# Performance work log

Hardware: AMD Instinct MI355X
Metric: run time of the kernel (lower is better)

## Reference

```python
import jax, jax.numpy as jnp
import numpy as np

B, T, I, H, L, C = 256, 512, 128, 256, 2, 1000


def _uniform(key, shape, k):
    return jax.random.uniform(key, shape, jnp.float32, -k, k)


def setup_inputs() -> dict:
    key = jax.random.key(0)
    ks = jax.random.split(key, 12)
    k = 1.0 / np.sqrt(H)
    return {
        "x": jax.random.normal(ks[0], (B, T, I), jnp.float32),
        # layer 0 (PyTorch LSTM param layout: W_ih [4H, in], W_hh [4H, H], biases [4H])
        "Wih0": _uniform(ks[1], (4 * H, I), k),
        "Whh0": _uniform(ks[2], (4 * H, H), k),
        "bih0": _uniform(ks[3], (4 * H,), k),
        "bhh0": _uniform(ks[4], (4 * H,), k),
        # layer 1
        "Wih1": _uniform(ks[5], (4 * H, H), k),
        "Whh1": _uniform(ks[6], (4 * H, H), k),
        "bih1": _uniform(ks[7], (4 * H,), k),
        "bhh1": _uniform(ks[8], (4 * H,), k),
        # final classifier
        "fcW": _uniform(ks[9], (C, H), k),
        "fcb": _uniform(ks[10], (C,), k),
    }


def _lstm_layer(seq, Wih, Whh, bias):
    # seq: [B, T, in]; returns hidden sequence [B, T, H]
    b, t = seq.shape[0], seq.shape[1]
    h_dim = Whh.shape[1]
    # Precompute input projection for all timesteps (one big GEMM).
    x_proj = jnp.einsum('bti,gi->btg', seq, Wih) + bias  # [B, T, 4H]

    def step(carry, xp):
        h, c = carry
        gates = xp + h @ Whh.T                     # [B, 4H]
        i, f, g, o = jnp.split(gates, 4, axis=-1)  # PyTorch gate order i,f,g,o
        i = jax.nn.sigmoid(i)
        f = jax.nn.sigmoid(f)
        g = jnp.tanh(g)
        o = jax.nn.sigmoid(o)
        c = f * c + i * g
        h = o * jnp.tanh(c)
        return (h, c), h

    h0 = jnp.zeros((b, h_dim), seq.dtype)
    c0 = jnp.zeros((b, h_dim), seq.dtype)
    _, hs = jax.lax.scan(step, (h0, c0), jnp.swapaxes(x_proj, 0, 1))  # [T, B, H]
    return jnp.swapaxes(hs, 0, 1)


def reference(x, Wih0, Whh0, bih0, bhh0, Wih1, Whh1, bih1, bhh1, fcW, fcb):
    out = _lstm_layer(x, Wih0, Whh0, bih0 + bhh0)
    out = _lstm_layer(out, Wih1, Whh1, bih1 + bhh1)
    # classifier on last timestep
    return out[:, -1, :] @ fcW.T + fcb  # [B, C]
```

## Files before the change

kernel.cpp:

```cpp
#include <hip/hip_runtime.h>

#define B_ 256
#define T_ 512
#define I_ 128
#define H_ 256
#define C_ 1000

__device__ __forceinline__ float fsig(float x) { return 1.0f / (1.0f + __expf(-x)); }
__device__ __forceinline__ float ftanh(float x) { return 2.0f / (1.0f + __expf(-2.0f * x)) - 1.0f; }

__global__ __launch_bounds__(256) void lstm_step(
    const float* __restrict__ x,
    const float* __restrict__ Wih0, const float* __restrict__ Whh0,
    const float* __restrict__ bih0, const float* __restrict__ bhh0,
    const float* __restrict__ Wih1, const float* __restrict__ Whh1,
    const float* __restrict__ bih1, const float* __restrict__ bhh1,
    float* __restrict__ ws, int s)
{
    __shared__ float As[128 * 36];
    __shared__ float Wsh[128 * 36];

    float* h0buf = ws;
    float* h1buf = ws + 2 * B_ * H_;
    float* c0 = ws + 4 * B_ * H_;
    float* c1 = ws + 5 * B_ * H_;

    const int w = blockIdx.x;
    const int layer = w >> 8;
    const int r = w & 255;
    const int bb = r >> 5;
    const int hb = r & 31;

    if (layer == 0 && s >= T_) return;
    if (layer == 1 && s < 1) return;
    const int t = (layer == 0) ? s : (s - 1);

    const float* hprev; const float* h0cur = nullptr;
    float* hout; float* cbuf;
    const float* Wih; const float* Whh; const float* bi; const float* bh;
    int nchunks;
    if (layer == 0) {
        hprev = h0buf + ((t - 1) & 1) * B_ * H_;
        hout  = h0buf + (t & 1) * B_ * H_;
        cbuf = c0; Wih = Wih0; Whh = Whh0; bi = bih0; bh = bhh0;
        nchunks = 3;
    } else {
        h0cur = h0buf + (t & 1) * B_ * H_;
        hprev = h1buf + ((t - 1) & 1) * B_ * H_;
        hout  = h1buf + (t & 1) * B_ * H_;
        cbuf = c1; Wih = Wih1; Whh = Whh1; bi = bih1; bh = bhh1;
        nchunks = 4;
    }

    const int tid = threadIdx.x;
    const int srow = tid >> 3;
    const int kv = tid & 7;
    const int wave = tid >> 6;
    const int lane = tid & 63;
    const int br = lane >> 3;
    const int gc8 = lane & 7;
    const int grow = (srow >> 3) * H_ + hb * 8 + (srow & 7);

    float acc[4][4];
#pragma unroll
    for (int a = 0; a < 4; ++a)
#pragma unroll
        for (int b = 0; b < 4; ++b) acc[a][b] = 0.0f;

    for (int cc = 0; cc < nchunks; ++cc) {
        const float* ap;
        const float* wp;
        if (layer == 0) {
            if (cc == 0) { ap = x + ((size_t)(bb * 32 + srow) * T_ + t) * I_; wp = Wih + grow * I_; }
            else         { ap = hprev + (bb * 32 + srow) * H_ + (cc - 1) * 128; wp = Whh + grow * H_ + (cc - 1) * 128; }
        } else {
            if (cc < 2)  { ap = h0cur + (bb * 32 + srow) * H_ + cc * 128;       wp = Wih + grow * H_ + cc * 128; }
            else         { ap = hprev + (bb * 32 + srow) * H_ + (cc - 2) * 128; wp = Whh + grow * H_ + (cc - 2) * 128; }
        }
#pragma unroll
        for (int i = 0; i < 4; ++i) {
            const int k4 = (kv + 8 * i) * 4;
            float4 va = *(const float4*)(ap + k4);
            As[(k4 + 0) * 36 + srow] = va.x;
            As[(k4 + 1) * 36 + srow] = va.y;
            As[(k4 + 2) * 36 + srow] = va.z;
            As[(k4 + 3) * 36 + srow] = va.w;
            float4 vw = *(const float4*)(wp + k4);
            Wsh[(k4 + 0) * 36 + srow] = vw.x;
            Wsh[(k4 + 1) * 36 + srow] = vw.y;
            Wsh[(k4 + 2) * 36 + srow] = vw.z;
            Wsh[(k4 + 3) * 36 + srow] = vw.w;
        }
        __syncthreads();
        const float* Ap = &As[(wave * 32) * 36 + br * 4];
        const float* Wp = &Wsh[(wave * 32) * 36 + gc8 * 4];
#pragma unroll
        for (int kk = 0; kk < 32; ++kk) {
            float4 a = *(const float4*)(Ap + kk * 36);
            float4 wv = *(const float4*)(Wp + kk * 36);
            acc[0][0] += a.x * wv.x; acc[0][1] += a.x * wv.y; acc[0][2] += a.x * wv.z; acc[0][3] += a.x * wv.w;
            acc[1][0] += a.y * wv.x; acc[1][1] += a.y * wv.y; acc[1][2] += a.y * wv.z; acc[1][3] += a.y * wv.w;
            acc[2][0] += a.z * wv.x; acc[2][1] += a.z * wv.y; acc[2][2] += a.z * wv.z; acc[2][3] += a.z * wv.w;
            acc[3][0] += a.w * wv.x; acc[3][1] += a.w * wv.y; acc[3][2] += a.w * wv.z; acc[3][3] += a.w * wv.w;
        }
        __syncthreads();
    }

    float* red = As;
    {
        const int base = tid * 16;
#pragma unroll
        for (int a = 0; a < 4; ++a)
#pragma unroll
            for (int b = 0; b < 4; ++b)
                red[base + a * 4 + b] = acc[a][b];
    }
    __syncthreads();
    {
        const int bl = tid >> 3;
        const int j = tid & 7;
        float g4[4];
#pragma unroll
        for (int g = 0; g < 4; ++g) {
            const int gc = g * 8 + j;
            const int br2 = bl >> 2, bi2 = bl & 3, gq = gc >> 2, gj = gc & 3;
            float v = 0.0f;
#pragma unroll
            for (int wv = 0; wv < 4; ++wv)
                v += red[(wv * 64 + br2 * 8 + gq) * 16 + bi2 * 4 + gj];
            const int growg = g * H_ + hb * 8 + j;
            v += bi[growg] + bh[growg];
            g4[g] = v;
        }
        const float ig = fsig(g4[0]);
        const float fg = fsig(g4[1]);
        const float gg = ftanh(g4[2]);
        const float og = fsig(g4[3]);
        const int b = bb * 32 + bl;
        const int hidx = hb * 8 + j;
        const int ci = b * H_ + hidx;
        const float cn = fg * cbuf[ci] + ig * gg;
        cbuf[ci] = cn;
        hout[ci] = og * ftanh(cn);
    }
}

__global__ __launch_bounds__(256) void fc_kernel(
    const float* __restrict__ ws, const float* __restrict__ fcW,
    const float* __restrict__ fcb, float* __restrict__ out)
{
    __shared__ float As[128 * 36];
    __shared__ float Wsh[128 * 36];

    const float* h1 = ws + 3 * B_ * H_;
    const int bb = blockIdx.x >> 5;
    const int cb = blockIdx.x & 31;
    const int tid = threadIdx.x;
    const int srow = tid >> 3;
    const int kv = tid & 7;
    const int wave = tid >> 6;
    const int lane = tid & 63;
    const int br = lane >> 3;
    const int gc8 = lane & 7;
    const int crow = cb * 32 + srow;

    float acc[4][4];
#pragma unroll
    for (int a = 0; a < 4; ++a)
#pragma unroll
        for (int b = 0; b < 4; ++b) acc[a][b] = 0.0f;

    for (int cc = 0; cc < 2; ++cc) {
        const float* ap = h1 + (bb * 32 + srow) * H_ + cc * 128;
#pragma unroll
        for (int i = 0; i < 4; ++i) {
            const int k4 = (kv + 8 * i) * 4;
            float4 va = *(const float4*)(ap + k4);
            As[(k4 + 0) * 36 + srow] = va.x;
            As[(k4 + 1) * 36 + srow] = va.y;
            As[(k4 + 2) * 36 + srow] = va.z;
            As[(k4 + 3) * 36 + srow] = va.w;
            float4 vw = make_float4(0.f, 0.f, 0.f, 0.f);
            if (crow < C_) vw = *(const float4*)(fcW + crow * H_ + cc * 128 + k4);
            Wsh[(k4 + 0) * 36 + srow] = vw.x;
            Wsh[(k4 + 1) * 36 + srow] = vw.y;
            Wsh[(k4 + 2) * 36 + srow] = vw.z;
            Wsh[(k4 + 3) * 36 + srow] = vw.w;
        }
        __syncthreads();
        const float* Ap = &As[(wave * 32) * 36 + br * 4];
        const float* Wp = &Wsh[(wave * 32) * 36 + gc8 * 4];
#pragma unroll
        for (int kk = 0; kk < 32; ++kk) {
            float4 a = *(const float4*)(Ap + kk * 36);
            float4 wv = *(const float4*)(Wp + kk * 36);
            acc[0][0] += a.x * wv.x; acc[0][1] += a.x * wv.y; acc[0][2] += a.x * wv.z; acc[0][3] += a.x * wv.w;
            acc[1][0] += a.y * wv.x; acc[1][1] += a.y * wv.y; acc[1][2] += a.y * wv.z; acc[1][3] += a.y * wv.w;
            acc[2][0] += a.z * wv.x; acc[2][1] += a.z * wv.y; acc[2][2] += a.z * wv.z; acc[2][3] += a.z * wv.w;
            acc[3][0] += a.w * wv.x; acc[3][1] += a.w * wv.y; acc[3][2] += a.w * wv.z; acc[3][3] += a.w * wv.w;
        }
        __syncthreads();
    }

    float* red = As;
    {
        const int base = tid * 16;
#pragma unroll
        for (int a = 0; a < 4; ++a)
#pragma unroll
            for (int b = 0; b < 4; ++b)
                red[base + a * 4 + b] = acc[a][b];
    }
    __syncthreads();
    {
        const int bl = tid >> 3;
        const int j = tid & 7;
#pragma unroll
        for (int g = 0; g < 4; ++g) {
            const int gc = g * 8 + j;
            const int br2 = bl >> 2, bi2 = bl & 3, gq = gc >> 2, gj = gc & 3;
            float v = 0.0f;
#pragma unroll
            for (int wv = 0; wv < 4; ++wv)
                v += red[(wv * 64 + br2 * 8 + gq) * 16 + bi2 * 4 + gj];
            const int cglob = cb * 32 + gc;
            if (cglob < C_) {
                v += fcb[cglob];
                out[(size_t)(bb * 32 + bl) * C_ + cglob] = v;
            }
        }
    }
}

extern "C" void kernel_launch(void* const* d_in, const int* in_sizes, int n_in,
                              void* d_out, int out_size, void* d_ws, size_t ws_size,
                              hipStream_t stream)
{
    const float* x    = (const float*)d_in[0];
    const float* Wih0 = (const float*)d_in[1];
    const float* Whh0 = (const float*)d_in[2];
    const float* bih0 = (const float*)d_in[3];
    const float* bhh0 = (const float*)d_in[4];
    const float* Wih1 = (const float*)d_in[5];
    const float* Whh1 = (const float*)d_in[6];
    const float* bih1 = (const float*)d_in[7];
    const float* bhh1 = (const float*)d_in[8];
    const float* fcW  = (const float*)d_in[9];
    const float* fcb  = (const float*)d_in[10];
    float* ws  = (float*)d_ws;
    float* out = (float*)d_out;

    hipMemsetAsync(d_ws, 0, (size_t)6 * B_ * H_ * sizeof(float), stream);

    for (int s = 0; s <= T_; ++s) {
        lstm_step<<<512, 256, 0, stream>>>(x, Wih0, Whh0, bih0, bhh0,
                                           Wih1, Whh1, bih1, bhh1, ws, s);
    }
    fc_kernel<<<256, 256, 0, stream>>>(ws, fcW, fcb, out);
}
```

Measured before the change: 7.486 ms.

## Replace per-timestep kernel launches with persistent kernel and per-batch-group barriers

Merges the 513 per-step launches and the classifier launch into one persistent kernel of 512 blocks. Blocks sharing a batch group sync through an atomic counter barrier with sleep polling, and hidden state is passed through agent-scope atomic loads and stores. This removes launch overhead and the device-wide step boundary, so batch groups can run ahead independently. The cost is that all 512 blocks must be co-resident, which relies on 2 blocks per CU, or the kernel deadlocks. It also adds spin overhead and relaxed-ordering risks.

Measured after the change: 8.458 ms. +13.0%, slower.

```diff
diff --git a/kernel.cpp b/kernel.cpp
--- a/kernel.cpp
+++ b/kernel.cpp
@@ -9,13 +9,23 @@
 __device__ __forceinline__ float fsig(float x) { return 1.0f / (1.0f + __expf(-x)); }
 __device__ __forceinline__ float ftanh(float x) { return 2.0f / (1.0f + __expf(-2.0f * x)) - 1.0f; }
 
-__global__ __launch_bounds__(256) void lstm_step(
+__device__ __forceinline__ float4 load_f4_coh(const float* p) {
+    unsigned long long* q = (unsigned long long*)p;
+    unsigned long long a = __hip_atomic_load(&q[0], __ATOMIC_RELAXED, __HIP_MEMORY_SCOPE_AGENT);
+    unsigned long long b = __hip_atomic_load(&q[1], __ATOMIC_RELAXED, __HIP_MEMORY_SCOPE_AGENT);
+    union { unsigned long long u; float f[2]; } ua, ub;
+    ua.u = a; ub.u = b;
+    return make_float4(ua.f[0], ua.f[1], ub.f[0], ub.f[1]);
+}
+
+__global__ __launch_bounds__(256, 2) void lstm_persistent(
     const float* __restrict__ x,
     const float* __restrict__ Wih0, const float* __restrict__ Whh0,
     const float* __restrict__ bih0, const float* __restrict__ bhh0,
     const float* __restrict__ Wih1, const float* __restrict__ Whh1,
     const float* __restrict__ bih1, const float* __restrict__ bhh1,
-    float* __restrict__ ws, int s)
+    const float* __restrict__ fcW, const float* __restrict__ fcb,
+    float* __restrict__ ws, float* __restrict__ out)
 {
     __shared__ float As[128 * 36];
     __shared__ float Wsh[128 * 36];
@@ -24,33 +34,14 @@
     float* h1buf = ws + 2 * B_ * H_;
     float* c0 = ws + 4 * B_ * H_;
     float* c1 = ws + 5 * B_ * H_;
+    unsigned* cnts = (unsigned*)(ws + 6 * B_ * H_);
 
     const int w = blockIdx.x;
     const int layer = w >> 8;
     const int r = w & 255;
     const int bb = r >> 5;
     const int hb = r & 31;
-
-    if (layer == 0 && s >= T_) return;
-    if (layer == 1 && s < 1) return;
-    const int t = (layer == 0) ? s : (s - 1);
-
-    const float* hprev; const float* h0cur = nullptr;
-    float* hout; float* cbuf;
-    const float* Wih; const float* Whh; const float* bi; const float* bh;
-    int nchunks;
-    if (layer == 0) {
-        hprev = h0buf + ((t - 1) & 1) * B_ * H_;
-        hout  = h0buf + (t & 1) * B_ * H_;
-        cbuf = c0; Wih = Wih0; Whh = Whh0; bi = bih0; bh = bhh0;
-        nchunks = 3;
-    } else {
-        h0cur = h0buf + (t & 1) * B_ * H_;
-        hprev = h1buf + ((t - 1) & 1) * B_ * H_;
-        hout  = h1buf + (t & 1) * B_ * H_;
-        cbuf = c1; Wih = Wih1; Whh = Whh1; bi = bih1; bh = bhh1;
-        nchunks = 4;
-    }
+    unsigned* cnt = cnts + bb * 64;
 
     const int tid = threadIdx.x;
     const int srow = tid >> 3;
@@ -61,172 +52,198 @@
     const int gc8 = lane & 7;
     const int grow = (srow >> 3) * H_ + hb * 8 + (srow & 7);
 
-    float acc[4][4];
-#pragma unroll
-    for (int a = 0; a < 4; ++a)
-#pragma unroll
-        for (int b = 0; b < 4; ++b) acc[a][b] = 0.0f;
-
-    for (int cc = 0; cc < nchunks; ++cc) {
-        const float* ap;
-        const float* wp;
-        if (layer == 0) {
-            if (cc == 0) { ap = x + ((size_t)(bb * 32 + srow) * T_ + t) * I_; wp = Wih + grow * I_; }
-            else         { ap = hprev + (bb * 32 + srow) * H_ + (cc - 1) * 128; wp = Whh + grow * H_ + (cc - 1) * 128; }
-        } else {
-            if (cc < 2)  { ap = h0cur + (bb * 32 + srow) * H_ + cc * 128;       wp = Wih + grow * H_ + cc * 128; }
-            else         { ap = hprev + (bb * 32 + srow) * H_ + (cc - 2) * 128; wp = Whh + grow * H_ + (cc - 2) * 128; }
-        }
-#pragma unroll
-        for (int i = 0; i < 4; ++i) {
-            const int k4 = (kv + 8 * i) * 4;
-            float4 va = *(const float4*)(ap + k4);
-            As[(k4 + 0) * 36 + srow] = va.x;
-            As[(k4 + 1) * 36 + srow] = va.y;
-            As[(k4 + 2) * 36 + srow] = va.z;
-            As[(k4 + 3) * 36 + srow] = va.w;
-            float4 vw = *(const float4*)(wp + k4);
-            Wsh[(k4 + 0) * 36 + srow] = vw.x;
-            Wsh[(k4 + 1) * 36 + srow] = vw.y;
-            Wsh[(k4 + 2) * 36 + srow] = vw.z;
-            Wsh[(k4 + 3) * 36 + srow] = vw.w;
-        }
+    const float* Wih = layer ? Wih1 : Wih0;
+    const float* Whh = layer ? Whh1 : Whh0;
+    const float* bi  = layer ? bih1 : bih0;
+    const float* bh  = layer ? bhh1 : bhh0;
+    const int nchunks = layer ? 4 : 3;
+
+    for (int s = 0; s <= T_; ++s) {
+        const bool active = layer ? (s >= 1) : (s < T_);
+        if (active) {
+            const int t = layer ? (s - 1) : s;
+            const float* hprev;
+            const float* h0cur = nullptr;
+            float* hout;
+            float* cbuf;
+            if (layer == 0) {
+                hprev = h0buf + ((t - 1) & 1) * B_ * H_;
+                hout  = h0buf + (t & 1) * B_ * H_;
+                cbuf = c0;
+            } else {
+                h0cur = h0buf + (t & 1) * B_ * H_;
+                hprev = h1buf + ((t - 1) & 1) * B_ * H_;
+                hout  = h1buf + (t & 1) * B_ * H_;
+                cbuf = c1;
+            }
+
+            float acc[4][4];
+#pragma unroll
+            for (int a = 0; a < 4; ++a)
+#pragma unroll
+                for (int b = 0; b < 4; ++b) acc[a][b] = 0.0f;
+
+            for (int cc = 0; cc < nchunks; ++cc) {
+                const float* ap;
+                const float* wp;
+                bool ap_coherent = true;
+                if (layer == 0) {
+                    if (cc == 0) { ap = x + ((size_t)(bb * 32 + srow) * T_ + t) * I_; wp = Wih + grow * I_; ap_coherent = false; }
+                    else         { ap = hprev + (bb * 32 + srow) * H_ + (cc - 1) * 128; wp = Whh + grow * H_ + (cc - 1) * 128; }
+                } else {
+                    if (cc < 2)  { ap = h0cur + (bb * 32 + srow) * H_ + cc * 128;       wp = Wih + grow * H_ + cc * 128; }
+                    else         { ap = hprev + (bb * 32 + srow) * H_ + (cc - 2) * 128; wp = Whh + grow * H_ + (cc - 2) * 128; }
+                }
+#pragma unroll
+                for (int i = 0; i < 4; ++i) {
+                    const int k4 = (kv + 8 * i) * 4;
+                    float4 va = ap_coherent ? load_f4_coh(ap + k4) : *(const float4*)(ap + k4);
+                    As[(k4 + 0) * 36 + srow] = va.x;
+                    As[(k4 + 1) * 36 + srow] = va.y;
+                    As[(k4 + 2) * 36 + srow] = va.z;
+                    As[(k4 + 3) * 36 + srow] = va.w;
+                    float4 vw = *(const float4*)(wp + k4);
+                    Wsh[(k4 + 0) * 36 + srow] = vw.x;
+                    Wsh[(k4 + 1) * 36 + srow] = vw.y;
+                    Wsh[(k4 + 2) * 36 + srow] = vw.z;
+                    Wsh[(k4 + 3) * 36 + srow] = vw.w;
+                }
+                __syncthreads();
+                const float* Ap = &As[(wave * 32) * 36 + br * 4];
+                const float* Wp = &Wsh[(wave * 32) * 36 + gc8 * 4];
+#pragma unroll
+                for (int kk = 0; kk < 32; ++kk) {
+                    float4 a = *(const float4*)(Ap + kk * 36);
+                    float4 wv = *(const float4*)(Wp + kk * 36);
+                    acc[0][0] += a.x * wv.x; acc[0][1] += a.x * wv.y; acc[0][2] += a.x * wv.z; acc[0][3] += a.x * wv.w;
+                    acc[1][0] += a.y * wv.x; acc[1][1] += a.y * wv.y; acc[1][2] += a.y * wv.z; acc[1][3] += a.y * wv.w;
+                    acc[2][0] += a.z * wv.x; acc[2][1] += a.z * wv.y; acc[2][2] += a.z * wv.z; acc[2][3] += a.z * wv.w;
+                    acc[3][0] += a.w * wv.x; acc[3][1] += a.w * wv.y; acc[3][2] += a.w * wv.z; acc[3][3] += a.w * wv.w;
+                }
+                __syncthreads();
+            }
+
+            float* red = As;
+            {
+                const int base = tid * 16;
+#pragma unroll
+                for (int a = 0; a < 4; ++a)
+#pragma unroll
+                    for (int b = 0; b < 4; ++b)
+                        red[base + a * 4 + b] = acc[a][b];
+            }
+            __syncthreads();
+            {
+                const int bl = tid >> 3;
+                const int j = tid & 7;
+                float g4[4];
+#pragma unroll
+                for (int g = 0; g < 4; ++g) {
+                    const int gc = g * 8 + j;
+                    const int br2 = bl >> 2, bi2 = bl & 3, gq = gc >> 2, gj = gc & 3;
+                    float v = 0.0f;
+#pragma unroll
+                    for (int wv = 0; wv < 4; ++wv)
+                        v += red[(wv * 64 + br2 * 8 + gq) * 16 + bi2 * 4 + gj];
+                    const int growg = g * H_ + hb * 8 + j;
+                    v += bi[growg] + bh[growg];
+                    g4[g] = v;
+                }
+                const float ig = fsig(g4[0]);
+                const float fg = fsig(g4[1]);
+                const float gg = ftanh(g4[2]);
+                const float og = fsig(g4[3]);
+                const int b = bb * 32 + bl;
+                const int hidx = hb * 8 + j;
+                const int ci = b * H_ + hidx;
+                const float cn = fg * cbuf[ci] + ig * gg;
+                cbuf[ci] = cn;
+                __hip_atomic_store(&hout[ci], og * ftanh(cn),
+                                   __ATOMIC_RELAXED, __HIP_MEMORY_SCOPE_AGENT);
+            }
+            __syncthreads();
+        }
+
         __syncthreads();
-        const float* Ap = &As[(wave * 32) * 36 + br * 4];
-        const float* Wp = &Wsh[(wave * 32) * 36 + gc8 * 4];
-#pragma unroll
-        for (int kk = 0; kk < 32; ++kk) {
-            float4 a = *(const float4*)(Ap + kk * 36);
-            float4 wv = *(const float4*)(Wp + kk * 36);
-            acc[0][0] += a.x * wv.x; acc[0][1] += a.x * wv.y; acc[0][2] += a.x * wv.z; acc[0][3] += a.x * wv.w;
-            acc[1][0] += a.y * wv.x; acc[1][1] += a.y * wv.y; acc[1][2] += a.y * wv.z; acc[1][3] += a.y * wv.w;
-            acc[2][0] += a.z * wv.x; acc[2][1] += a.z * wv.y; acc[2][2] += a.z * wv.z; acc[2][3] += a.z * wv.w;
-            acc[3][0] += a.w * wv.x; acc[3][1] += a.w * wv.y; acc[3][2] += a.w * wv.z; acc[3][3] += a.w * wv.w;
+        if (tid == 0) {
+            __hip_atomic_fetch_add(cnt, 1u, __ATOMIC_RELAXED, __HIP_MEMORY_SCOPE_AGENT);
+            const unsigned target = (unsigned)(s + 1) * 64u;
+            while (__hip_atomic_load(cnt, __ATOMIC_RELAXED, __HIP_MEMORY_SCOPE_AGENT) < target) {
+                __builtin_amdgcn_s_sleep(2);
+            }
         }
         __syncthreads();
     }
 
-    float* red = As;
-    {
-        const int base = tid * 16;
+    if (layer == 1) {
+        const int cb = hb;
+        const float* h1 = ws + 3 * B_ * H_;
+        const int crow = cb * 32 + srow;
+
+        float acc[4][4];
 #pragma unroll
         for (int a = 0; a < 4; ++a)
 #pragma unroll
-            for (int b = 0; b < 4; ++b)
-                red[base + a * 4 + b] = acc[a][b];
-    }
-    __syncthreads();
-    {
-        const int bl = tid >> 3;
-        const int j = tid & 7;
-        float g4[4];
-#pragma unroll
-        for (int g = 0; g < 4; ++g) {
-            const int gc = g * 8 + j;
-            const int br2 = bl >> 2, bi2 = bl & 3, gq = gc >> 2, gj = gc & 3;
-            float v = 0.0f;
-#pragma unroll
-            for (int wv = 0; wv < 4; ++wv)
-                v += red[(wv * 64 + br2 * 8 + gq) * 16 + bi2 * 4 + gj];
-            const int growg = g * H_ + hb * 8 + j;
-            v += bi[growg] + bh[growg];
-            g4[g] = v;
-        }
-        const float ig = fsig(g4[0]);
-        const float fg = fsig(g4[1]);
-        const float gg = ftanh(g4[2]);
-        const float og = fsig(g4[3]);
-        const int b = bb * 32 + bl;
-        const int hidx = hb * 8 + j;
-        const int ci = b * H_ + hidx;
-        const float cn = fg * cbuf[ci] + ig * gg;
-        cbuf[ci] = cn;
-        hout[ci] = og * ftanh(cn);
-    }
-}
-
-__global__ __launch_bounds__(256) void fc_kernel(
-    const float* __restrict__ ws, const float* __restrict__ fcW,
-    const float* __restrict__ fcb, float* __restrict__ out)
-{
-    __shared__ float As[128 * 36];
-    __shared__ float Wsh[128 * 36];
-
-    const float* h1 = ws + 3 * B_ * H_;
-    const int bb = blockIdx.x >> 5;
-    const int cb = blockIdx.x & 31;
-    const int tid = threadIdx.x;
-    const int srow = tid >> 3;
-    const int kv = tid & 7;
-    const int wave = tid >> 6;
-    const int lane = tid & 63;
-    const int br = lane >> 3;
-    const int gc8 = lane & 7;
-    const int crow = cb * 32 + srow;
-
-    float acc[4][4];
-#pragma unroll
-    for (int a = 0; a < 4; ++a)
-#pragma unroll
-        for (int b = 0; b < 4; ++b) acc[a][b] = 0.0f;
-
-    for (int cc = 0; cc < 2; ++cc) {
-        const float* ap = h1 + (bb * 32 + srow) * H_ + cc * 128;
-#pragma unroll
-        for (int i = 0; i < 4; ++i) {
-            const int k4 = (kv + 8 * i) * 4;
-            float4 va = *(const float4*)(ap + k4);
-            As[(k4 + 0) * 36 + srow] = va.x;
-            As[(k4 + 1) * 36 + srow] = va.y;
-            As[(k4 + 2) * 36 + srow] = va.z;
-            As[(k4 + 3) * 36 + srow] = va.w;
-            float4 vw = make_float4(0.f, 0.f, 0.f, 0.f);
-            if (crow < C_) vw = *(const float4*)(fcW + crow * H_ + cc * 128 + k4);
-            Wsh[(k4 + 0) * 36 + srow] = vw.x;
-            Wsh[(k4 + 1) * 36 + srow] = vw.y;
-            Wsh[(k4 + 2) * 36 + srow] = vw.z;
-            Wsh[(k4 + 3) * 36 + srow] = vw.w;
+            for (int b = 0; b < 4; ++b) acc[a][b] = 0.0f;
+
+        for (int cc = 0; cc < 2; ++cc) {
+            const float* ap = h1 + (bb * 32 + srow) * H_ + cc * 128;
+#pragma unroll
+            for (int i = 0; i < 4; ++i) {
+                const int k4 = (kv + 8 * i) * 4;
+                float4 va = load_f4_coh(ap + k4);
+                As[(k4 + 0) * 36 + srow] = va.x;
+                As[(k4 + 1) * 36 + srow] = va.y;
+                As[(k4 + 2) * 36 + srow] = va.z;
+                As[(k4 + 3) * 36 + srow] = va.w;
+                float4 vw = make_float4(0.f, 0.f, 0.f, 0.f);
+                if (crow < C_) vw = *(const float4*)(fcW + crow * H_ + cc * 128 + k4);
+                Wsh[(k4 + 0) * 36 + srow] = vw.x;
+                Wsh[(k4 + 1) * 36 + srow] = vw.y;
+                Wsh[(k4 + 2) * 36 + srow] = vw.z;
+                Wsh[(k4 + 3) * 36 + srow] = vw.w;
+            }
+            __syncthreads();
+            const float* Ap = &As[(wave * 32) * 36 + br * 4];
+            const float* Wp = &Wsh[(wave * 32) * 36 + gc8 * 4];
+#pragma unroll
+            for (int kk = 0; kk < 32; ++kk) {
+                float4 a = *(const float4*)(Ap + kk * 36);
+                float4 wv = *(const float4*)(Wp + kk * 36);
+                acc[0][0] += a.x * wv.x; acc[0][1] += a.x * wv.y; acc[0][2] += a.x * wv.z; acc[0][3] += a.x * wv.w;
+                acc[1][0] += a.y * wv.x; acc[1][1] += a.y * wv.y; acc[1][2] += a.y * wv.z; acc[1][3] += a.y * wv.w;
+                acc[2][0] += a.z * wv.x; acc[2][1] += a.z * wv.y; acc[2][2] += a.z * wv.z; acc[2][3] += a.z * wv.w;
+                acc[3][0] += a.w * wv.x; acc[3][1] += a.w * wv.y; acc[3][2] += a.w * wv.z; acc[3][3] += a.w * wv.w;
+            }
+            __syncthreads();
+        }
+
+        float* red = As;
+        {
+            const int base = tid * 16;
+#pragma unroll
+            for (int a = 0; a < 4; ++a)
+#pragma unroll
+                for (int b = 0; b < 4; ++b)
+                    red[base + a * 4 + b] = acc[a][b];
         }
         __syncthreads();
-        const float* Ap = &As[(wave * 32) * 36 + br * 4];
-        const float* Wp = &Wsh[(wave * 32) * 36 + gc8 * 4];
-#pragma unroll
-        for (int kk = 0; kk < 32; ++kk) {
-            float4 a = *(const float4*)(Ap + kk * 36);
-            float4 wv = *(const float4*)(Wp + kk * 36);
-            acc[0][0] += a.x * wv.x; acc[0][1] += a.x * wv.y; acc[0][2] += a.x * wv.z; acc[0][3] += a.x * wv.w;
-            acc[1][0] += a.y * wv.x; acc[1][1] += a.y * wv.y; acc[1][2] += a.y * wv.z; acc[1][3] += a.y * wv.w;
-            acc[2][0] += a.z * wv.x; acc[2][1] += a.z * wv.y; acc[2][2] += a.z * wv.z; acc[2][3] += a.z * wv.w;
-            acc[3][0] += a.w * wv.x; acc[3][1] += a.w * wv.y; acc[3][2] += a.w * wv.z; acc[3][3] += a.w * wv.w;
-        }
-        __syncthreads();
-    }
-
-    float* red = As;
-    {
-        const int base = tid * 16;
-#pragma unroll
-        for (int a = 0; a < 4; ++a)
-#pragma unroll
-            for (int b = 0; b < 4; ++b)
-                red[base + a * 4 + b] = acc[a][b];
-    }
-    __syncthreads();
-    {
-        const int bl = tid >> 3;
-        const int j = tid & 7;
-#pragma unroll
-        for (int g = 0; g < 4; ++g) {
-            const int gc = g * 8 + j;
-            const int br2 = bl >> 2, bi2 = bl & 3, gq = gc >> 2, gj = gc & 3;
-            float v = 0.0f;
-#pragma unroll
-            for (int wv = 0; wv < 4; ++wv)
-                v += red[(wv * 64 + br2 * 8 + gq) * 16 + bi2 * 4 + gj];
-            const int cglob = cb * 32 + gc;
-            if (cglob < C_) {
-                v += fcb[cglob];
-                out[(size_t)(bb * 32 + bl) * C_ + cglob] = v;
+        {
+            const int bl = tid >> 3;
+            const int j = tid & 7;
+#pragma unroll
+            for (int g = 0; g < 4; ++g) {
+                const int gc = g * 8 + j;
+                const int br2 = bl >> 2, bi2 = bl & 3, gq = gc >> 2, gj = gc & 3;
+                float v = 0.0f;
+#pragma unroll
+                for (int wv = 0; wv < 4; ++wv)
+                    v += red[(wv * 64 + br2 * 8 + gq) * 16 + bi2 * 4 + gj];
+                const int cglob = cb * 32 + gc;
+                if (cglob < C_) {
+                    v += fcb[cglob];
+                    out[(size_t)(bb * 32 + bl) * C_ + cglob] = v;
+                }
             }
         }
     }
@@ -250,11 +267,8 @@
     float* ws  = (float*)d_ws;
     float* out = (float*)d_out;
 
-    hipMemsetAsync(d_ws, 0, (size_t)6 * B_ * H_ * sizeof(float), stream);
-
-    for (int s = 0; s <= T_; ++s) {
-        lstm_step<<<512, 256, 0, stream>>>(x, Wih0, Whh0, bih0, bhh0,
-                                           Wih1, Whh1, bih1, bhh1, ws, s);
-    }
-    fc_kernel<<<256, 256, 0, stream>>>(ws, fcW, fcb, out);
+    hipMemsetAsync(d_ws, 0, (size_t)(6 * B_ * H_ + 8 * 64) * sizeof(float), stream);
+
+    lstm_persistent<<<512, 256, 0, stream>>>(
+        x, Wih0, Whh0, bih0, bhh0, Wih1, Whh1, bih1, bhh1, fcW, fcb, ws, out);
 }
```
